# Kernel tuning notes

Measured on AMD Instinct MI355X. Metric: run time of the kernel, lower is better.

The kernel has to match this reference:

```python
import jax, jax.numpy as jnp
import numpy as np

MAX_POS = 1024  # config.max_position_embeddings
NUM_HEADS = 16
HEAD_DIM = 64


def setup_inputs() -> dict:
    key = jax.random.key(0)
    ks = jax.random.split(key, 4)
    B, S, H = 4, 1024, 1024
    return {
        "hidden_states": jax.random.normal(ks[0], (B, S, H), dtype=jnp.float32),
        "qkv_w": jax.random.normal(ks[1], (3 * H, H), dtype=jnp.float32) * 0.02,
        "qkv_b": jax.random.normal(ks[2], (3 * H,), dtype=jnp.float32) * 0.02,
        "dist_emb": jax.random.normal(ks[3], (2 * MAX_POS - 1, HEAD_DIM), dtype=jnp.float32) * 0.02,
        "ext_mask": jnp.zeros((B, 1, 1, S), dtype=jnp.float32),
    }


def reference(hidden_states, qkv_w, qkv_b, dist_emb, ext_mask):
    B, S, H = hidden_states.shape
    h, d = NUM_HEADS, HEAD_DIM
    # fused QKV projection (q|k|v concatenated on output dim)
    qkv = jnp.einsum('bsi,oi->bso', hidden_states, qkv_w) + qkv_b
    q, k, v = jnp.split(qkv, 3, axis=-1)
    to_heads = lambda x: x.reshape(B, S, h, d).transpose(0, 2, 1, 3)  # [B,h,S,d]
    q, k, v = to_heads(q), to_heads(k), to_heads(v)
    # raw attention scores [B,h,S,S]
    scores = jnp.einsum('bhld,bhrd->bhlr', q, k)
    # relative_key_query positional bias
    pos = jnp.arange(S)
    distance = pos[:, None] - pos[None, :]          # [S,S]
    pe = dist_emb[distance + MAX_POS - 1]           # [S,S,d]
    scores = scores + jnp.einsum('bhld,lrd->bhlr', q, pe) \
                    + jnp.einsum('bhrd,lrd->bhlr', k, pe)
    scores = scores / jnp.sqrt(jnp.asarray(d, scores.dtype))
    scores = scores + ext_mask
    probs = jax.nn.softmax(scores, axis=-1)
    ctx = jnp.einsum('bhlr,bhrd->bhld', probs, v)   # [B,h,S,d]
    return ctx.transpose(0, 2, 1, 3).reshape(B, S, h * d)
```

## Files before the change

kernel.cpp:

```cpp
#include <hip/hip_runtime.h>

#define SEQ 1024
#define NH  16

typedef __attribute__((ext_vector_type(8))) short short8;
typedef __attribute__((ext_vector_type(4))) float floatx4;
typedef __attribute__((ext_vector_type(4))) unsigned short ushortx4;

#define GLDS16(gp, lp) __builtin_amdgcn_global_load_lds( \
    (const __attribute__((address_space(1))) void*)(gp), \
    (__attribute__((address_space(3))) void*)(lp), 16, 0, 0)

__device__ __forceinline__ unsigned short f2b(float f) {
    union { float f; unsigned u; } v; v.f = f;
    unsigned r = (v.u + 0x7fffu + ((v.u >> 16) & 1u)) >> 16;
    return (unsigned short)r;
}
__device__ __forceinline__ float b2f(unsigned short h) {
    union { unsigned u; float f; } v; v.u = ((unsigned)h) << 16;
    return v.f;
}

#define TADDR(base, row, ch) ((base) + ((row) << 6) + ((((ch) ^ ((row) & 7))) << 3))
#define UWADDR(dl, x) (((dl) << 6) + ((((x) >> 2) ^ ((dl) & 15)) << 2) + ((x) & 3))

__global__ void cast_kernel(const float* __restrict__ hs, const float* __restrict__ W,
                            const float* __restrict__ E,
                            unsigned short* __restrict__ hsb,
                            unsigned short* __restrict__ Wb,
                            unsigned short* __restrict__ Eb)
{
    const int QH = 1048576, QW = 786432, QE = 32752;
    const int NT = QH + QW + QE;
    for (int q = blockIdx.x * 256 + threadIdx.x; q < NT; q += gridDim.x * 256) {
        const float* src; unsigned short* dst; int off;
        if (q < QH)           { src = hs; dst = hsb; off = q; }
        else if (q < QH + QW) { src = W;  dst = Wb;  off = q - QH; }
        else                  { src = E;  dst = Eb;  off = q - QH - QW; }
        const float4 v = *(const float4*)(src + (size_t)off * 4);
        ushortx4 o; o[0] = f2b(v.x); o[1] = f2b(v.y); o[2] = f2b(v.z); o[3] = f2b(v.w);
        *(ushortx4*)(dst + (size_t)off * 4) = o;
    }
}

__global__ __launch_bounds__(256, 3) void qkv_gemm(
    const unsigned short* __restrict__ Ab, const unsigned short* __restrict__ Bb,
    const float* __restrict__ bias,
    unsigned short* __restrict__ Qb, unsigned short* __restrict__ Kb,
    unsigned short* __restrict__ Vt)
{
    __shared__ unsigned short sm[8192];
    const int t = threadIdx.x, w = t >> 6;
    const int ln = t & 15, g = (t >> 4) & 3;
    const int wm = w >> 1, wn = w & 1;
    const int m0 = blockIdx.y << 7, o0 = blockIdx.x << 7;

    floatx4 acc[4][4];
#pragma unroll
    for (int i = 0; i < 4; ++i)
#pragma unroll
        for (int j = 0; j < 4; ++j) acc[i][j] = (floatx4){0.f, 0.f, 0.f, 0.f};

    auto stage = [&](int kb) {
#pragma unroll
        for (int p = 0; p < 2; ++p) {
            const int idx = (p << 8) + t;
            const int row = idx >> 2;
            const int c = (idx & 3) ^ ((row ^ (row >> 2)) & 3);
            GLDS16(Ab + (size_t)(m0 + row) * 1024 + kb + (c << 3),
                   (char*)sm + (p << 12) + (w << 10));
            GLDS16(Bb + (size_t)(o0 + row) * 1024 + kb + (c << 3),
                   (char*)sm + 8192 + (p << 12) + (w << 10));
        }
    };

    stage(0);
    for (int kb = 0;;) {
        __syncthreads();
        short8 af[4], bf_[4];
#pragma unroll
        for (int i = 0; i < 4; ++i) {
            const int r = (wm << 6) + (i << 4) + ln;
            af[i] = *(const short8*)&sm[(r << 5) + ((g ^ ((r ^ (r >> 2)) & 3)) << 3)];
        }
#pragma unroll
        for (int j = 0; j < 4; ++j) {
            const int r = (wn << 6) + (j << 4) + ln;
            bf_[j] = *(const short8*)&sm[4096 + (r << 5) + ((g ^ ((r ^ (r >> 2)) & 3)) << 3)];
        }
#pragma unroll
        for (int i = 0; i < 4; ++i)
#pragma unroll
            for (int j = 0; j < 4; ++j)
                acc[i][j] = __builtin_amdgcn_mfma_f32_16x16x32_bf16(af[i], bf_[j], acc[i][j], 0, 0, 0);
        kb += 32;
        if (kb >= 1024) break;
        __syncthreads();
        stage(kb);
    }

    const int which = o0 >> 10;
    float bj[4];
#pragma unroll
    for (int j = 0; j < 4; ++j) bj[j] = bias[o0 + (wn << 6) + (j << 4) + ln];

    if (which == 2) {
#pragma unroll
        for (int i = 0; i < 4; ++i) {
            const int m = m0 + (wm << 6) + (i << 4) + (g << 2);
            const int b = m >> 10, s = m & 1023;
#pragma unroll
            for (int j = 0; j < 4; ++j) {
                const int o = o0 + (wn << 6) + (j << 4) + ln;
                const int d = o & 63, hh = (o >> 6) & 15;
                ushortx4 pk;
#pragma unroll
                for (int q = 0; q < 4; ++q) pk[q] = f2b(acc[i][j][q] + bj[j]);
                *(ushortx4*)(Vt + (((size_t)((b << 4) + hh)) << 16) + (d << 10) + s) = pk;
            }
        }
    } else {
        unsigned short* dst = which ? Kb : Qb;
        const float sc = which ? 1.0f : 0.125f;
#pragma unroll
        for (int i = 0; i < 4; ++i)
#pragma unroll
            for (int q = 0; q < 4; ++q) {
                const int m = m0 + (wm << 6) + (i << 4) + (g << 2) + q;
                const int b = m >> 10, s = m & 1023;
#pragma unroll
                for (int j = 0; j < 4; ++j) {
                    const int o = o0 + (wn << 6) + (j << 4) + ln;
                    const int d = o & 63, hh = (o >> 6) & 15;
                    dst[(((size_t)((b << 4) + hh)) << 16) + (s << 6) + d] =
                        f2b((acc[i][j][q] + bj[j]) * sc);
                }
            }
    }
}

__global__ __launch_bounds__(256, 2) void attn_mfma(
    const unsigned short* __restrict__ Qb, const unsigned short* __restrict__ Kb,
    const unsigned short* __restrict__ Vt, const unsigned short* __restrict__ Eb,
    const float* __restrict__ mask, float* __restrict__ outp)
{
    __shared__ unsigned short sm[32768];
    const int t = threadIdx.x, w = t >> 6;
    const int ln = t & 15, g = (t >> 4) & 3;
    const int bh = blockIdx.x >> 4;
    const int l0 = (blockIdx.x & 15) << 6;
    const int b = bh >> 4, h = bh & 15;
    const size_t hb = (size_t)bh << 16;
    const int x0 = (w << 4) + (g << 2);

#pragma unroll
    for (int p = 0; p < 2; ++p) {
        const int idx = (p << 8) + t;
        const int row = idx >> 3;
        const int c = (idx & 7) ^ (row & 7);
        GLDS16(Qb + hb + ((size_t)(l0 + row) << 6) + (c << 3),
               (char*)sm + (p << 12) + (w << 10));
    }

    floatx4 O[4];
    float mr[4], lr[4];
#pragma unroll
    for (int dt = 0; dt < 4; ++dt) O[dt] = (floatx4){0.f, 0.f, 0.f, 0.f};
#pragma unroll
    for (int q = 0; q < 4; ++q) { mr[q] = -1e30f; lr[q] = 0.f; }

    short8 qa0, qa1;

    for (int r0 = 0; r0 < SEQ; r0 += 64) {
        __syncthreads();
#pragma unroll
        for (int p = 0; p < 2; ++p) {
            const int idx = (p << 8) + t;
            const int row = idx >> 3;
            const int c = (idx & 7) ^ (row & 7);
            GLDS16(Kb + hb + ((size_t)(r0 + row) << 6) + (c << 3),
                   (char*)sm + 8192 + (p << 12) + (w << 10));
        }
        const int j0 = l0 - r0 + 960;
#pragma unroll
        for (int p = 0; p < 4; ++p) {
            const int idx = (p << 8) + t;
            const int row = idx >> 3;
            const int c = (idx & 7) ^ (row & 7);
            GLDS16(Eb + ((size_t)(j0 + row) << 6) + (c << 3),
                   (char*)sm + 16384 + (p << 12) + (w << 10));
        }
        __syncthreads();
        if (r0 == 0) {
            const int qr = (w << 4) + ln;
            qa0 = *(const short8*)&sm[TADDR(0, qr, g)];
            qa1 = *(const short8*)&sm[TADDR(0, qr, 4 + g)];
        }
        short8 kf[4][2];
#pragma unroll
        for (int j = 0; j < 4; ++j) {
            const int kr = (j << 4) + ln;
            kf[j][0] = *(const short8*)&sm[TADDR(4096, kr, g)];
            kf[j][1] = *(const short8*)&sm[TADDR(4096, kr, 4 + g)];
        }
        const int wr = (w << 4) + ln;
        const short8 ka0 = *(const short8*)&sm[TADDR(4096, wr, g)];
        const short8 ka1 = *(const short8*)&sm[TADDR(4096, wr, 4 + g)];

        floatx4 S[4];
#pragma unroll
        for (int j = 0; j < 4; ++j) {
            floatx4 z = (floatx4){0.f, 0.f, 0.f, 0.f};
            z = __builtin_amdgcn_mfma_f32_16x16x32_bf16(qa0, kf[j][0], z, 0, 0, 0);
            S[j] = __builtin_amdgcn_mfma_f32_16x16x32_bf16(qa1, kf[j][1], z, 0, 0, 0);
        }
#pragma unroll
        for (int dt = 0; dt < 8; ++dt) {
            const int er = (dt << 4) + ln;
            const short8 e0 = *(const short8*)&sm[TADDR(8192, er, g)];
            const short8 e1 = *(const short8*)&sm[TADDR(8192, er, 4 + g)];
            floatx4 z = (floatx4){0.f, 0.f, 0.f, 0.f};
            z = __builtin_amdgcn_mfma_f32_16x16x32_bf16(qa0, e0, z, 0, 0, 0);
            const floatx4 U = __builtin_amdgcn_mfma_f32_16x16x32_bf16(qa1, e1, z, 0, 0, 0);
            floatx4 z2 = (floatx4){0.f, 0.f, 0.f, 0.f};
            z2 = __builtin_amdgcn_mfma_f32_16x16x32_bf16(ka0, e0, z2, 0, 0, 0);
            const floatx4 Wv = __builtin_amdgcn_mfma_f32_16x16x32_bf16(ka1, e1, z2, 0, 0, 0);
            ushortx4 up, wp;
#pragma unroll
            for (int q = 0; q < 4; ++q) { up[q] = f2b(U[q]); wp[q] = f2b(Wv[q] * 0.125f); }
            const int dl = (dt << 4) + ln;
            *(ushortx4*)&sm[16384 + UWADDR(dl, x0)] = up;
            *(ushortx4*)&sm[24576 + UWADDR(dl, x0)] = wp;
        }
        __syncthreads();
#pragma unroll
        for (int p = 0; p < 2; ++p) {
            const int idx = (p << 8) + t;
            const int row = idx >> 3;
            const int c = (idx & 7) ^ (row & 7);
            GLDS16(Vt + hb + ((size_t)row << 10) + r0 + (c << 3),
                   (char*)sm + 16384 + (p << 12) + (w << 10));
        }
        float Pw[4][4];
#pragma unroll
        for (int j = 0; j < 4; ++j) {
            const int rr = (j << 4) + ln;
            const float mk = mask[(b << 10) + r0 + rr];
#pragma unroll
            for (int q = 0; q < 4; ++q) {
                const int l = x0 + q;
                const int dl = l - rr + 63;
                S[j][q] += b2f(sm[16384 + UWADDR(dl, l)]) +
                           b2f(sm[24576 + UWADDR(dl, rr)]) + mk;
            }
        }
#pragma unroll
        for (int q = 0; q < 4; ++q) {
            float tm = fmaxf(fmaxf(S[0][q], S[1][q]), fmaxf(S[2][q], S[3][q]));
            tm = fmaxf(tm, __shfl_xor(tm, 1));
            tm = fmaxf(tm, __shfl_xor(tm, 2));
            tm = fmaxf(tm, __shfl_xor(tm, 4));
            tm = fmaxf(tm, __shfl_xor(tm, 8));
            const float mnew = fmaxf(mr[q], tm);
            const float al = __expf(mr[q] - mnew);
            float sum = 0.f;
#pragma unroll
            for (int j = 0; j < 4; ++j) {
                const float p = __expf(S[j][q] - mnew);
                Pw[j][q] = p; sum += p;
            }
            sum += __shfl_xor(sum, 1);
            sum += __shfl_xor(sum, 2);
            sum += __shfl_xor(sum, 4);
            sum += __shfl_xor(sum, 8);
            lr[q] = lr[q] * al + sum;
            mr[q] = mnew;
#pragma unroll
            for (int dt = 0; dt < 4; ++dt) O[dt][q] *= al;
        }
#pragma unroll
        for (int j = 0; j < 4; ++j) {
            const int rr = (j << 4) + ln;
#pragma unroll
            for (int q = 0; q < 4; ++q) {
                const int l = x0 + q;
                sm[12288 + (l << 6) + ((((rr >> 3) ^ (l & 7)) << 3)) + (rr & 7)] = f2b(Pw[j][q]);
            }
        }
        __syncthreads();
        const int pr = (w << 4) + ln;
        const short8 pa0 = *(const short8*)&sm[TADDR(12288, pr, g)];
        const short8 pa1 = *(const short8*)&sm[TADDR(12288, pr, 4 + g)];
#pragma unroll
        for (int dt = 0; dt < 4; ++dt) {
            const int vr = (dt << 4) + ln;
            const short8 v0 = *(const short8*)&sm[TADDR(8192, vr, g)];
            const short8 v1 = *(const short8*)&sm[TADDR(8192, vr, 4 + g)];
            O[dt] = __builtin_amdgcn_mfma_f32_16x16x32_bf16(pa0, v0, O[dt], 0, 0, 0);
            O[dt] = __builtin_amdgcn_mfma_f32_16x16x32_bf16(pa1, v1, O[dt], 0, 0, 0);
        }
    }
#pragma unroll
    for (int dt = 0; dt < 4; ++dt)
#pragma unroll
        for (int q = 0; q < 4; ++q) {
            const int l = x0 + q;
            outp[((size_t)b << 20) + ((size_t)(l0 + l) << 10) + (h << 6) + (dt << 4) + ln]
                = O[dt][q] / lr[q];
        }
}

extern "C" void kernel_launch(void* const* d_in, const int* in_sizes, int n_in,
                              void* d_out, int out_size, void* d_ws, size_t ws_size,
                              hipStream_t stream)
{
    const float* hs   = (const float*)d_in[0];
    const float* qkvw = (const float*)d_in[1];
    const float* qkvb = (const float*)d_in[2];
    const float* demb = (const float*)d_in[3];
    const float* mask = (const float*)d_in[4];
    float* out = (float*)d_out;

    char* ws = (char*)d_ws;
    unsigned short* hsb = (unsigned short*)(ws);
    unsigned short* Wb  = (unsigned short*)(ws + 8388608);
    unsigned short* Eb  = (unsigned short*)(ws + 14680064);
    unsigned short* Qb  = (unsigned short*)(ws + 14942208);
    unsigned short* Kb  = (unsigned short*)(ws + 23330816);
    unsigned short* Vt  = (unsigned short*)(ws + 31719424);

    cast_kernel<<<2048, 256, 0, stream>>>(hs, qkvw, demb, hsb, Wb, Eb);
    qkv_gemm<<<dim3(24, 32), 256, 0, stream>>>(hsb, Wb, qkvb, Qb, Kb, Vt);
    attn_mfma<<<1024, 256, 0, stream>>>(Qb, Kb, Vt, Eb, mask, out);
}
```

Measured before the change: 240.1 us.

## Skip unused relative-position MFMA tiles, compact LDS layout, swizzle blocks

Each wave now computes only the distance-embedding tiles its 16 query rows actually need for the U and W bias terms, skipping the rest of the 8-tile sweep. The U/W results are written into skewed, diagonal-indexed LDS buffers so the bias can be read back as one vector load per row. Q fragments are loaded straight from global memory instead of staged through LDS. Together these shrink shared memory to about 50KB, so launch bounds rise to 3 blocks per CU, and block IDs are swizzled to change L2 locality. The cost is more complex index arithmetic, wave-dependent branching inside the unrolled loop, and possible register pressure at higher occupancy.

```diff
diff --git a/kernel.cpp b/kernel.cpp
--- a/kernel.cpp
+++ b/kernel.cpp
@@ -22,7 +22,6 @@
 }
 
 #define TADDR(base, row, ch) ((base) + ((row) << 6) + ((((ch) ^ ((row) & 7))) << 3))
-#define UWADDR(dl, x) (((dl) << 6) + ((((x) >> 2) ^ ((dl) & 15)) << 2) + ((x) & 3))
 
 __global__ void cast_kernel(const float* __restrict__ hs, const float* __restrict__ W,
                             const float* __restrict__ E,
@@ -139,28 +138,26 @@
     }
 }
 
-__global__ __launch_bounds__(256, 2) void attn_mfma(
+__global__ __launch_bounds__(256, 3) void attn_mfma(
     const unsigned short* __restrict__ Qb, const unsigned short* __restrict__ Kb,
     const unsigned short* __restrict__ Vt, const unsigned short* __restrict__ Eb,
     const float* __restrict__ mask, float* __restrict__ outp)
 {
-    __shared__ unsigned short sm[32768];
+    __shared__ __align__(16) unsigned short sm[25600];
     const int t = threadIdx.x, w = t >> 6;
+    const int wu = __builtin_amdgcn_readfirstlane(w);
     const int ln = t & 15, g = (t >> 4) & 3;
-    const int bh = blockIdx.x >> 4;
-    const int l0 = (blockIdx.x & 15) << 6;
+    const int bid = blockIdx.x;
+    const int swz = ((bid & 7) << 7) | (bid >> 3);
+    const int bh = swz >> 4;
+    const int l0 = (swz & 15) << 6;
     const int b = bh >> 4, h = bh & 15;
     const size_t hb = (size_t)bh << 16;
     const int x0 = (w << 4) + (g << 2);
 
-#pragma unroll
-    for (int p = 0; p < 2; ++p) {
-        const int idx = (p << 8) + t;
-        const int row = idx >> 3;
-        const int c = (idx & 7) ^ (row & 7);
-        GLDS16(Qb + hb + ((size_t)(l0 + row) << 6) + (c << 3),
-               (char*)sm + (p << 12) + (w << 10));
-    }
+    const int qr = (w << 4) + ln;
+    const short8 qa0 = *(const short8*)(Qb + hb + ((size_t)(l0 + qr) << 6) + (g << 3));
+    const short8 qa1 = *(const short8*)(Qb + hb + ((size_t)(l0 + qr) << 6) + 32 + (g << 3));
 
     floatx4 O[4];
     float mr[4], lr[4];
@@ -168,8 +165,6 @@
     for (int dt = 0; dt < 4; ++dt) O[dt] = (floatx4){0.f, 0.f, 0.f, 0.f};
 #pragma unroll
     for (int q = 0; q < 4; ++q) { mr[q] = -1e30f; lr[q] = 0.f; }
-
-    short8 qa0, qa1;
 
     for (int r0 = 0; r0 < SEQ; r0 += 64) {
         __syncthreads();
@@ -179,7 +174,7 @@
             const int row = idx >> 3;
             const int c = (idx & 7) ^ (row & 7);
             GLDS16(Kb + hb + ((size_t)(r0 + row) << 6) + (c << 3),
-                   (char*)sm + 8192 + (p << 12) + (w << 10));
+                   (char*)sm + (p << 12) + (w << 10));
         }
         const int j0 = l0 - r0 + 960;
 #pragma unroll
@@ -188,24 +183,19 @@
             const int row = idx >> 3;
             const int c = (idx & 7) ^ (row & 7);
             GLDS16(Eb + ((size_t)(j0 + row) << 6) + (c << 3),
-                   (char*)sm + 16384 + (p << 12) + (w << 10));
-        }
-        __syncthreads();
-        if (r0 == 0) {
-            const int qr = (w << 4) + ln;
-            qa0 = *(const short8*)&sm[TADDR(0, qr, g)];
-            qa1 = *(const short8*)&sm[TADDR(0, qr, 4 + g)];
-        }
+                   (char*)sm + 8192 + (p << 12) + (w << 10));
+        }
+        __syncthreads();
         short8 kf[4][2];
 #pragma unroll
         for (int j = 0; j < 4; ++j) {
             const int kr = (j << 4) + ln;
-            kf[j][0] = *(const short8*)&sm[TADDR(4096, kr, g)];
-            kf[j][1] = *(const short8*)&sm[TADDR(4096, kr, 4 + g)];
+            kf[j][0] = *(const short8*)&sm[TADDR(0, kr, g)];
+            kf[j][1] = *(const short8*)&sm[TADDR(0, kr, 4 + g)];
         }
         const int wr = (w << 4) + ln;
-        const short8 ka0 = *(const short8*)&sm[TADDR(4096, wr, g)];
-        const short8 ka1 = *(const short8*)&sm[TADDR(4096, wr, 4 + g)];
+        const short8 ka0 = *(const short8*)&sm[TADDR(0, wr, g)];
+        const short8 ka1 = *(const short8*)&sm[TADDR(0, wr, 4 + g)];
 
         floatx4 S[4];
 #pragma unroll
@@ -216,21 +206,28 @@
         }
 #pragma unroll
         for (int dt = 0; dt < 8; ++dt) {
+            const bool doU = (dt >= wu) && (dt <= wu + 4);
+            const bool doW = (dt >= 3 - wu) && (dt <= 7 - wu);
+            if (!doU && !doW) continue;
             const int er = (dt << 4) + ln;
-            const short8 e0 = *(const short8*)&sm[TADDR(8192, er, g)];
-            const short8 e1 = *(const short8*)&sm[TADDR(8192, er, 4 + g)];
-            floatx4 z = (floatx4){0.f, 0.f, 0.f, 0.f};
-            z = __builtin_amdgcn_mfma_f32_16x16x32_bf16(qa0, e0, z, 0, 0, 0);
-            const floatx4 U = __builtin_amdgcn_mfma_f32_16x16x32_bf16(qa1, e1, z, 0, 0, 0);
-            floatx4 z2 = (floatx4){0.f, 0.f, 0.f, 0.f};
-            z2 = __builtin_amdgcn_mfma_f32_16x16x32_bf16(ka0, e0, z2, 0, 0, 0);
-            const floatx4 Wv = __builtin_amdgcn_mfma_f32_16x16x32_bf16(ka1, e1, z2, 0, 0, 0);
-            ushortx4 up, wp;
-#pragma unroll
-            for (int q = 0; q < 4; ++q) { up[q] = f2b(U[q]); wp[q] = f2b(Wv[q] * 0.125f); }
-            const int dl = (dt << 4) + ln;
-            *(ushortx4*)&sm[16384 + UWADDR(dl, x0)] = up;
-            *(ushortx4*)&sm[24576 + UWADDR(dl, x0)] = wp;
+            const short8 e0 = *(const short8*)&sm[TADDR(4096, er, g)];
+            const short8 e1 = *(const short8*)&sm[TADDR(4096, er, 4 + g)];
+            if (doU) {
+                floatx4 z = (floatx4){0.f, 0.f, 0.f, 0.f};
+                z = __builtin_amdgcn_mfma_f32_16x16x32_bf16(qa0, e0, z, 0, 0, 0);
+                const floatx4 U = __builtin_amdgcn_mfma_f32_16x16x32_bf16(qa1, e1, z, 0, 0, 0);
+                int a = 12288 + (x0 - (dt << 4) - ln + 79) * 72 + x0;
+#pragma unroll
+                for (int q = 0; q < 4; ++q) { sm[a] = f2b(U[q]); a += 73; }
+            }
+            if (doW) {
+                floatx4 z2 = (floatx4){0.f, 0.f, 0.f, 0.f};
+                z2 = __builtin_amdgcn_mfma_f32_16x16x32_bf16(ka0, e0, z2, 0, 0, 0);
+                const floatx4 Wv = __builtin_amdgcn_mfma_f32_16x16x32_bf16(ka1, e1, z2, 0, 0, 0);
+                int a = 19200 + x0 * 101 + (dt << 4) + ln - 47;
+#pragma unroll
+                for (int q = 0; q < 4; ++q) { sm[a] = f2b(Wv[q] * 0.125f); a += 101; }
+            }
         }
         __syncthreads();
 #pragma unroll
@@ -239,20 +236,18 @@
             const int row = idx >> 3;
             const int c = (idx & 7) ^ (row & 7);
             GLDS16(Vt + hb + ((size_t)row << 10) + r0 + (c << 3),
-                   (char*)sm + 16384 + (p << 12) + (w << 10));
+                   (char*)sm + 8192 + (p << 12) + (w << 10));
         }
         float Pw[4][4];
 #pragma unroll
         for (int j = 0; j < 4; ++j) {
             const int rr = (j << 4) + ln;
             const float mk = mask[(b << 10) + r0 + rr];
-#pragma unroll
-            for (int q = 0; q < 4; ++q) {
-                const int l = x0 + q;
-                const int dl = l - rr + 63;
-                S[j][q] += b2f(sm[16384 + UWADDR(dl, l)]) +
-                           b2f(sm[24576 + UWADDR(dl, rr)]) + mk;
-            }
+            const ushortx4 u4 = *(const ushortx4*)&sm[12288 + (rr + 16) * 72 + x0];
+            const ushortx4 w4 = *(const ushortx4*)&sm[19200 + rr * 100 + 16 + x0];
+#pragma unroll
+            for (int q = 0; q < 4; ++q)
+                S[j][q] += b2f(u4[q]) + b2f(w4[q]) + mk;
         }
 #pragma unroll
         for (int q = 0; q < 4; ++q) {
@@ -284,18 +279,18 @@
 #pragma unroll
             for (int q = 0; q < 4; ++q) {
                 const int l = x0 + q;
-                sm[12288 + (l << 6) + ((((rr >> 3) ^ (l & 7)) << 3)) + (rr & 7)] = f2b(Pw[j][q]);
+                sm[8192 + (l << 6) + ((((rr >> 3) ^ (l & 7)) << 3)) + (rr & 7)] = f2b(Pw[j][q]);
             }
         }
         __syncthreads();
         const int pr = (w << 4) + ln;
-        const short8 pa0 = *(const short8*)&sm[TADDR(12288, pr, g)];
-        const short8 pa1 = *(const short8*)&sm[TADDR(12288, pr, 4 + g)];
+        const short8 pa0 = *(const short8*)&sm[TADDR(8192, pr, g)];
+        const short8 pa1 = *(const short8*)&sm[TADDR(8192, pr, 4 + g)];
 #pragma unroll
         for (int dt = 0; dt < 4; ++dt) {
             const int vr = (dt << 4) + ln;
-            const short8 v0 = *(const short8*)&sm[TADDR(8192, vr, g)];
-            const short8 v1 = *(const short8*)&sm[TADDR(8192, vr, 4 + g)];
+            const short8 v0 = *(const short8*)&sm[TADDR(4096, vr, g)];
+            const short8 v1 = *(const short8*)&sm[TADDR(4096, vr, 4 + g)];
             O[dt] = __builtin_amdgcn_mfma_f32_16x16x32_bf16(pa0, v0, O[dt], 0, 0, 0);
             O[dt] = __builtin_amdgcn_mfma_f32_16x16x32_bf16(pa1, v1, O[dt], 0, 0, 0);
         }
```

New measurement: 230.2 us. -4.1%, faster.
